# Kernel tuning notes

Hardware: AMD Instinct MI355X
Metric: run time of the kernel (lower is better)

The kernel has to match this reference:

```python
import jax, jax.numpy as jnp
import numpy as np

B, N, F_IN, F_OUT = 16, 1024, 128, 128

def setup_inputs() -> dict:
    key = jax.random.key(0)
    k1, k2, k3 = jax.random.split(key, 3)
    X = jax.random.normal(k1, (B, N, F_IN), dtype=jnp.float32)
    A = jax.random.uniform(k2, (B, N, N), dtype=jnp.float32)
    W = jax.random.normal(k3, (F_IN, F_OUT), dtype=jnp.float32)
    return {"X": X, "A": A, "W": W}

def reference(X, A, W):
    # A_hat = A + I  (batched add of identity)
    n = A.shape[-1]
    A_hat = A + jnp.eye(n, dtype=A.dtype)  # [B,N,N]
    # D_hat^{-1/2} applied as elementwise row/col scaling (torch builds diag
    # matrices and inverts; mathematically identical for diagonal D).
    deg = jnp.sum(A_hat, axis=-1)               # [B,N]
    d_inv_sqrt = 1.0 / jnp.sqrt(deg)            # [B,N]
    A_norm = A_hat * d_inv_sqrt[:, :, None] * d_inv_sqrt[:, None, :]  # [B,N,N]
    out = jnp.einsum('bnm,bmf->bnf', A_norm, X)  # aggregation bmm
    out = jnp.einsum('bnf,fg->bng', out, W)      # weight matmul
    return out
```

## Files before the change

kernel.cpp:

```cpp
#include <hip/hip_runtime.h>

#define NN 1024
#define FF 128

typedef __attribute__((ext_vector_type(8))) short bf16x8;
typedef __attribute__((ext_vector_type(4))) float f32x4;

__device__ __forceinline__ unsigned short f2bf(float x) {
  unsigned u = __float_as_uint(x);
  u += 0x7fff + ((u >> 16) & 1);
  return (unsigned short)(u >> 16);
}
__device__ __forceinline__ float bf2f(unsigned short b) {
  return __uint_as_float(((unsigned)b) << 16);
}
__device__ __forceinline__ bf16x8 cvt8(float4 a, float4 b) {
  bf16x8 r;
  r[0] = (short)f2bf(a.x); r[1] = (short)f2bf(a.y);
  r[2] = (short)f2bf(a.z); r[3] = (short)f2bf(a.w);
  r[4] = (short)f2bf(b.x); r[5] = (short)f2bf(b.y);
  r[6] = (short)f2bf(b.z); r[7] = (short)f2bf(b.w);
  return r;
}

__device__ __forceinline__ void gl_lds16(const void* g, void* l) {
  __builtin_amdgcn_global_load_lds(
      (const __attribute__((address_space(1))) unsigned*)g,
      (__attribute__((address_space(3))) unsigned*)l, 16, 0, 0);
}

__global__ __launch_bounds__(256) void k_deg(const float* __restrict__ A,
                                             const float* __restrict__ W,
                                             float* __restrict__ d,
                                             unsigned short* __restrict__ Wt) {
  if (blockIdx.x >= 4096) {
    int id = (blockIdx.x - 4096) * 256 + threadIdx.x;
    int g = id >> 7, f = id & 127;
    Wt[g * 128 + f] = f2bf(W[f * 128 + g]);
    return;
  }
  int row  = blockIdx.x * 4 + (threadIdx.x >> 6);
  int lane = threadIdx.x & 63;
  const float4* Ar = (const float4*)(A + (size_t)row * NN);
  float s = 0.f;
#pragma unroll
  for (int i = 0; i < 4; ++i) {
    float4 v = Ar[lane + i * 64];
    s += (v.x + v.y) + (v.z + v.w);
  }
#pragma unroll
  for (int off = 32; off > 0; off >>= 1) s += __shfl_down(s, off, 64);
  if (lane == 0) d[row] = rsqrtf(s + 1.0f);
}

__global__ __launch_bounds__(256) void k_xw(const float* __restrict__ X,
                                            const unsigned short* __restrict__ Wt,
                                            const float* __restrict__ d,
                                            unsigned short* __restrict__ Yt) {
  __shared__ __align__(16) unsigned short Xs[64 * 128];
  __shared__ __align__(16) unsigned short Ws[128 * 128];
  __shared__ float dl[64];
  int t  = threadIdx.x;
  int b  = blockIdx.x >> 4;
  int m0 = (blockIdx.x & 15) * 64;

#pragma unroll
  for (int j = 0; j < 4; ++j) {
    int id = t + j * 256;
    int r = id >> 4, p = id & 15, c = p ^ (r & 15);
    const float* gp = X + ((size_t)(b * NN + m0 + r) * FF + c * 8);
    float4 v0 = *(const float4*)gp;
    float4 v1 = *(const float4*)(gp + 4);
    *(bf16x8*)&Xs[r * 128 + p * 8] = cvt8(v0, v1);
  }
#pragma unroll
  for (int j = 0; j < 8; ++j) {
    int id = t + j * 256;
    int g = id >> 4, p = id & 15, c = p ^ (g & 15);
    uint4 v = *(const uint4*)(Wt + g * 128 + c * 8);
    *(uint4*)&Ws[g * 128 + p * 8] = v;
  }
  if (t < 64) dl[t] = d[b * NN + m0 + t];
  __syncthreads();

  int wave = t >> 6, lane = t & 63, quad = lane >> 4, l16 = lane & 15;
  f32x4 acc[8];
#pragma unroll
  for (int ct = 0; ct < 8; ++ct) acc[ct] = (f32x4){0.f, 0.f, 0.f, 0.f};

#pragma unroll
  for (int ks = 0; ks < 4; ++ks) {
    int q = ks * 4 + quad;
    bf16x8 a = *(const bf16x8*)&Xs[(wave * 16 + l16) * 128 + (q ^ l16) * 8];
#pragma unroll
    for (int ct = 0; ct < 8; ++ct) {
      bf16x8 w = *(const bf16x8*)&Ws[(ct * 16 + l16) * 128 + (q ^ l16) * 8];
      acc[ct] = __builtin_amdgcn_mfma_f32_16x16x32_bf16(a, w, acc[ct], 0, 0, 0);
    }
  }

  int mb = wave * 16 + quad * 4;
  float4 d4 = *(const float4*)&dl[mb];
#pragma unroll
  for (int ct = 0; ct < 8; ++ct) {
    int g = ct * 16 + l16;
    ushort4 p;
    p.x = f2bf(d4.x * acc[ct][0]);
    p.y = f2bf(d4.y * acc[ct][1]);
    p.z = f2bf(d4.z * acc[ct][2]);
    p.w = f2bf(d4.w * acc[ct][3]);
    *(ushort4*)(Yt + (size_t)(b * 128 + g) * NN + m0 + mb) = p;
  }
}

__global__ __launch_bounds__(256) void k_agg(const float* __restrict__ A,
                                             const unsigned short* __restrict__ Yt,
                                             const float* __restrict__ d,
                                             float* __restrict__ out) {
  __shared__ __align__(16) float          Asf[32 * 128];
  __shared__ __align__(16) unsigned short Ys[128 * 128];
  int t   = threadIdx.x;
  int bid = blockIdx.x;
  int xcd = bid & 7;
  int j   = bid >> 3;
  int b   = xcd + 8 * (j >> 5);
  int n0  = (j & 31) * 32;
  int wave = t >> 6, lane = t & 63, quad = lane >> 4, l16 = lane & 15;
  int wr = wave >> 1, wc = wave & 1;
  int rl = lane >> 4, pl = lane & 15;
  int rh = lane >> 5, cc = lane & 31;

  const float*          Ab = A  + (size_t)(b * NN + n0) * NN;
  const unsigned short* Yb = Yt + (size_t)b * 128 * NN;

  auto issue = [&](int k0) {
#pragma unroll
    for (int jj = 0; jj < 4; ++jj) {
      int r0 = wave * 8 + jj * 2;
      int r  = r0 + rh;
      int c  = cc ^ (2 * (r & 15));
      gl_lds16(Ab + ((size_t)r * NN + k0 + c * 4), &Asf[r0 * 128]);
    }
#pragma unroll
    for (int jj = 0; jj < 8; ++jj) {
      int r0 = wave * 32 + jj * 4;
      int r  = r0 + rl;
      int c  = pl ^ (r & 15);
      gl_lds16(Yb + ((size_t)r * NN + k0 + c * 8), &Ys[r0 * 128]);
    }
  };

  f32x4 acc[4];
#pragma unroll
  for (int ct = 0; ct < 4; ++ct) acc[ct] = (f32x4){0.f, 0.f, 0.f, 0.f};

  int swA = 2 * l16;
  issue(0);
  for (int s = 0; s < 8; ++s) {
    __syncthreads();
#pragma unroll
    for (int ks = 0; ks < 4; ++ks) {
      int cq = ks * 4 + quad;
      int pa = (2 * cq) ^ swA;
      float4 a0 = *(const float4*)&Asf[(wr * 16 + l16) * 128 + pa * 4];
      float4 a1 = *(const float4*)&Asf[(wr * 16 + l16) * 128 + pa * 4 + 4];
      bf16x8 a = cvt8(a0, a1);
#pragma unroll
      for (int ct = 0; ct < 4; ++ct) {
        bf16x8 y = *(const bf16x8*)&Ys[(wc * 64 + ct * 16 + l16) * 128 + ((cq ^ l16)) * 8];
        acc[ct] = __builtin_amdgcn_mfma_f32_16x16x32_bf16(a, y, acc[ct], 0, 0, 0);
      }
    }
    __syncthreads();
    if (s < 7) issue((s + 1) * 128);
  }

  int nb = n0 + wr * 16 + quad * 4;
  float4 d4 = *(const float4*)(d + b * NN + nb);
#pragma unroll
  for (int ct = 0; ct < 4; ++ct) {
    int g = wc * 64 + ct * 16 + l16;
    ushort4 yv = *(const ushort4*)(Yt + (size_t)(b * 128 + g) * NN + nb);
    float* op = out + ((size_t)(b * NN + nb) * FF + g);
    op[0 * FF] = d4.x * (acc[ct][0] + bf2f(yv.x));
    op[1 * FF] = d4.y * (acc[ct][1] + bf2f(yv.y));
    op[2 * FF] = d4.z * (acc[ct][2] + bf2f(yv.z));
    op[3 * FF] = d4.w * (acc[ct][3] + bf2f(yv.w));
  }
}

extern "C" void kernel_launch(void* const* d_in, const int* in_sizes, int n_in,
                              void* d_out, int out_size, void* d_ws, size_t ws_size,
                              hipStream_t stream) {
  const float* X = (const float*)d_in[0];
  const float* A = (const float*)d_in[1];
  const float* W = (const float*)d_in[2];
  float* out = (float*)d_out;

  char* ws = (char*)d_ws;
  float*          dinv = (float*)ws;
  unsigned short* Wt   = (unsigned short*)(ws + 65536);
  unsigned short* Yt   = (unsigned short*)(ws + 98304);

  k_deg<<<dim3(4096 + 64), dim3(256), 0, stream>>>(A, W, dinv, Wt);
  k_xw <<<dim3(256),       dim3(256), 0, stream>>>(X, Wt, dinv, Yt);
  k_agg<<<dim3(512),       dim3(256), 0, stream>>>(A, Yt, dinv, out);
}
```

Measured before the change: 123.1 us.

## Triple-buffer k_agg LDS tiles with half-width K steps and vmcnt waits

Splits the aggregation K loop into 16 steps of 64 columns with three LDS buffers, so loads for two steps ahead are in flight while the current step computes. The two __syncthreads per step become one s_barrier after a partial s_waitcnt vmcnt, and the MFMA section is wrapped in s_setprio. The swizzle patterns change to match the 64-wide rows. In exchange there are more loop iterations and barriers, and correctness depends on the hand-chosen vmcnt count matching the number of loads issued per step and on a single barrier being enough to protect buffer reuse.

```diff
diff --git a/kernel.cpp b/kernel.cpp
--- a/kernel.cpp
+++ b/kernel.cpp
@@ -117,8 +117,8 @@
                                              const unsigned short* __restrict__ Yt,
                                              const float* __restrict__ d,
                                              float* __restrict__ out) {
-  __shared__ __align__(16) float          Asf[32 * 128];
-  __shared__ __align__(16) unsigned short Ys[128 * 128];
+  __shared__ __align__(16) float          Asf[3][32 * 64];
+  __shared__ __align__(16) unsigned short Ys[3][128 * 64];
   int t   = threadIdx.x;
   int bid = blockIdx.x;
   int xcd = bid & 7;
@@ -127,26 +127,25 @@
   int n0  = (j & 31) * 32;
   int wave = t >> 6, lane = t & 63, quad = lane >> 4, l16 = lane & 15;
   int wr = wave >> 1, wc = wave & 1;
-  int rl = lane >> 4, pl = lane & 15;
-  int rh = lane >> 5, cc = lane & 31;
 
   const float*          Ab = A  + (size_t)(b * NN + n0) * NN;
   const unsigned short* Yb = Yt + (size_t)b * 128 * NN;
 
-  auto issue = [&](int k0) {
+  int ra = lane >> 4, pa_s = lane & 15;
+  int ry_s = lane >> 3, py_s = lane & 7;
+
+  auto issue = [&](int k0, int bufi) {
+#pragma unroll
+    for (int jj = 0; jj < 2; ++jj) {
+      int r = wave * 8 + jj * 4 + ra;
+      int c = pa_s ^ (2 * (r & 7));
+      gl_lds16(Ab + ((size_t)r * NN + k0 + c * 4), &Asf[bufi][(wave * 8 + jj * 4) * 64]);
+    }
 #pragma unroll
     for (int jj = 0; jj < 4; ++jj) {
-      int r0 = wave * 8 + jj * 2;
-      int r  = r0 + rh;
-      int c  = cc ^ (2 * (r & 15));
-      gl_lds16(Ab + ((size_t)r * NN + k0 + c * 4), &Asf[r0 * 128]);
-    }
-#pragma unroll
-    for (int jj = 0; jj < 8; ++jj) {
-      int r0 = wave * 32 + jj * 4;
-      int r  = r0 + rl;
-      int c  = pl ^ (r & 15);
-      gl_lds16(Yb + ((size_t)r * NN + k0 + c * 8), &Ys[r0 * 128]);
+      int ry = wave * 32 + jj * 8 + ry_s;
+      int c  = py_s ^ (ry & 7);
+      gl_lds16(Yb + ((size_t)ry * NN + k0 + c * 8), &Ys[bufi][(wave * 32 + jj * 8) * 64]);
     }
   };
 
@@ -154,25 +153,35 @@
 #pragma unroll
   for (int ct = 0; ct < 4; ++ct) acc[ct] = (f32x4){0.f, 0.f, 0.f, 0.f};
 
-  int swA = 2 * l16;
-  issue(0);
-  for (int s = 0; s < 8; ++s) {
-    __syncthreads();
-#pragma unroll
-    for (int ks = 0; ks < 4; ++ks) {
+  int swA = 2 * (l16 & 7);
+  issue(0, 0);
+  issue(64, 1);
+
+#pragma unroll
+  for (int s = 0; s < 16; ++s) {
+    if (s < 15) asm volatile("s_waitcnt vmcnt(6)" ::: "memory");
+    else        asm volatile("s_waitcnt vmcnt(0)" ::: "memory");
+    __builtin_amdgcn_s_barrier();
+    const float*          as = &Asf[s % 3][0];
+    const unsigned short* ys = &Ys[s % 3][0];
+    __builtin_amdgcn_s_setprio(1);
+#pragma unroll
+    for (int ks = 0; ks < 2; ++ks) {
       int cq = ks * 4 + quad;
       int pa = (2 * cq) ^ swA;
-      float4 a0 = *(const float4*)&Asf[(wr * 16 + l16) * 128 + pa * 4];
-      float4 a1 = *(const float4*)&Asf[(wr * 16 + l16) * 128 + pa * 4 + 4];
+      float4 a0 = *(const float4*)&as[(wr * 16 + l16) * 64 + pa * 4];
+      float4 a1 = *(const float4*)&as[(wr * 16 + l16) * 64 + pa * 4 + 4];
       bf16x8 a = cvt8(a0, a1);
 #pragma unroll
       for (int ct = 0; ct < 4; ++ct) {
-        bf16x8 y = *(const bf16x8*)&Ys[(wc * 64 + ct * 16 + l16) * 128 + ((cq ^ l16)) * 8];
+        int cp = (cq ^ (l16 & 7)) * 8;
+        bf16x8 y = *(const bf16x8*)&ys[(wc * 64 + ct * 16 + l16) * 64 + cp];
         acc[ct] = __builtin_amdgcn_mfma_f32_16x16x32_bf16(a, y, acc[ct], 0, 0, 0);
       }
     }
-    __syncthreads();
-    if (s < 7) issue((s + 1) * 128);
+    __builtin_amdgcn_s_setprio(0);
+    __builtin_amdgcn_sched_barrier(0);
+    if (s < 14) issue((s + 2) * 64, (s + 2) % 3);
   }
 
   int nb = n0 + wr * 16 + quad * 4;
```

New measurement: 118.9 us. 3.5% less time.
